# Performance work log

Hardware: AMD Instinct MI355X
Metric: run time of the kernel (lower is better)

Reference implementation:

```python
import jax, jax.numpy as jnp
import numpy as np

B, S, D = 4, 2048, 1024


def setup_inputs() -> dict:
    key = jax.random.key(0)
    ks = jax.random.split(key, 4)
    scale = 1.0 / np.sqrt(D)
    x = jax.random.normal(ks[0], (B, S, D), dtype=jnp.float32)
    Wk = jax.random.normal(ks[1], (D, D), dtype=jnp.float32) * scale
    Wq = jax.random.normal(ks[2], (D, D), dtype=jnp.float32) * scale
    Wv = jax.random.normal(ks[3], (D, D), dtype=jnp.float32) * scale
    bk = jnp.zeros((D,), dtype=jnp.float32)
    bq = jnp.zeros((D,), dtype=jnp.float32)
    bv = jnp.zeros((D,), dtype=jnp.float32)
    return {"x": x, "Wk": Wk, "bk": bk, "Wq": Wq, "bq": bq,
            "Wv": Wv, "bv": bv, "dims": 2}


def correlated_weight(k, q, v, dims):
    # correlation between every query position and every key position,
    # scaled by sqrt(d) for numerical stability (standard correlation attn)
    d = q.shape[-1]
    scores = jnp.einsum("bqd,bkd->bqk", q, k) / jnp.sqrt(jnp.asarray(d, q.dtype))
    w = jax.nn.softmax(scores, axis=dims)          # [B, S, S]
    return jnp.einsum("bqk,bkd->bqd", w, v)        # [B, S, D]


def reference(x, Wk, bk, Wq, bq, Wv, bv, dims):
    # injected key/query/value funcs instantiated as Linear layers
    k = jnp.einsum("bsd,de->bse", x, Wk) + bk
    q = jnp.einsum("bsd,de->bse", x, Wq) + bq
    v = jnp.einsum("bsd,de->bse", x, Wv) + bv
    return correlated_weight(k, q, v, dims)
```

## Files before the change

### kernel.cpp

```cpp
#include <hip/hip_runtime.h>
#include <hip/hip_bf16.h>
#include <stdint.h>


typedef unsigned short u16;
typedef __bf16 bf16x8 __attribute__((ext_vector_type(8)));
typedef float  f32x4  __attribute__((ext_vector_type(4)));
typedef float  f32x16 __attribute__((ext_vector_type(16)));
typedef u16    u16x4  __attribute__((ext_vector_type(4)));
typedef u16    u16x8  __attribute__((ext_vector_type(8)));

__device__ __forceinline__ u16 f2bf(float f) {
  union { float f; uint32_t u; } v; v.f = f;
  uint32_t r = v.u + 0x7fffu + ((v.u >> 16) & 1u);
  return (u16)(r >> 16);
}
__device__ __forceinline__ float bf2f(u16 b) {
  union { uint32_t u; float f; } v; v.u = (uint32_t)b << 16; return v.f;
}

#define GLD_LDS16(gp, lp) __builtin_amdgcn_global_load_lds(                   \
    (const __attribute__((address_space(1))) void*)(gp),                      \
    (__attribute__((address_space(3))) void*)(lp), 16, 0, 0)


__global__ __launch_bounds__(256)
void prep_all(const float* __restrict__ x,
              const float* __restrict__ Wq, const float* __restrict__ Wk,
              const float* __restrict__ Wv,
              const float* __restrict__ bq, const float* __restrict__ bk,
              const float* __restrict__ bv,
              u16* __restrict__ xb, u16* __restrict__ wt,
              float* __restrict__ bc) {
  __shared__ float t[32][33];
  const int bid = blockIdx.x;
  if (bid < 4096) {
    int i = (bid * 256 + threadIdx.x) * 8;
    float4 v0 = *(const float4*)(x + i);
    float4 v1 = *(const float4*)(x + i + 4);
    u16x8 o;
    o[0] = f2bf(v0.x); o[1] = f2bf(v0.y); o[2] = f2bf(v0.z); o[3] = f2bf(v0.w);
    o[4] = f2bf(v1.x); o[5] = f2bf(v1.y); o[6] = f2bf(v1.z); o[7] = f2bf(v1.w);
    *(u16x8*)(xb + i) = o;
  } else if (bid < 4096 + 3072) {
    int b2 = bid - 4096;
    int z = b2 >> 10, rem = b2 & 1023;
    int e0 = (rem & 31) * 32, d0 = (rem >> 5) * 32;
    const float* W = z == 0 ? Wq : (z == 1 ? Wk : Wv);
    u16* dst = wt + (size_t)z * 1024 * 1024;
    int tx = threadIdx.x & 31, ty = threadIdx.x >> 5;
    #pragma unroll
    for (int i = 0; i < 4; ++i)
      t[ty + i * 8][tx] = W[(size_t)(d0 + ty + i * 8) * 1024 + e0 + tx];
    __syncthreads();
    #pragma unroll
    for (int i = 0; i < 4; ++i)
      dst[(size_t)(e0 + ty + i * 8) * 1024 + d0 + tx] =
          f2bf(t[tx][ty + i * 8]);
  } else {
    int i = (bid - 7168) * 256 + threadIdx.x;
    if (i < 3072)
      bc[i] = (i < 1024) ? bq[i] : (i < 2048 ? bk[i - 1024] : bv[i - 2048]);
  }
}


__global__ __launch_bounds__(256)
void gemm_v(const u16* __restrict__ A, int lda,
            const u16* __restrict__ B, int ldb,
            const float* __restrict__ bias, int K,
            u16* __restrict__ vTp) {
  __shared__ __align__(16) u16 smem[128 * 132];
  u16* As = smem;
  u16* Bs = smem + 8192;
  const int lane = threadIdx.x & 63;
  const int wv = threadIdx.x >> 6;

  const int flat = blockIdx.y * 8 + blockIdx.x;
  const int swz = (flat & 7) * 64 + (flat >> 3);
  const int bx = swz & 7, by = swz >> 3;

  const u16* Ab = A + (size_t)by * 128 * lda;
  const u16* Bb = B + (size_t)bx * 128 * ldb;

  const int srow = lane >> 3;
  const int scol = ((lane & 7) ^ (lane >> 3)) * 8;
  const int r32 = lane & 31;
  const int half = lane >> 5;
  const int rx = lane & 7;
  const int wm = (wv >> 1) * 64;
  const int wn = (wv & 1) * 64;

  f32x16 acc[2][2];
  #pragma unroll
  for (int i = 0; i < 2; ++i)
    #pragma unroll
    for (int j = 0; j < 2; ++j) acc[i][j] = (f32x16)0.0f;

  for (int k0 = 0; k0 < K; k0 += 64) {
    #pragma unroll
    for (int i = 0; i < 4; ++i) {
      int r = wv * 32 + i * 8;
      GLD_LDS16(Ab + (size_t)(r + srow) * lda + k0 + scol, As + r * 64);
      GLD_LDS16(Bb + (size_t)(r + srow) * ldb + k0 + scol, Bs + r * 64);
    }
    __syncthreads();

    bf16x8 af[2][4], bfr[2][4];
    #pragma unroll
    for (int i = 0; i < 2; ++i)
      #pragma unroll
      for (int t = 0; t < 4; ++t) {
        int pc = ((t * 2 + half) ^ rx) * 8;
        af[i][t]  = *(const bf16x8*)(As + (wm + i * 32 + r32) * 64 + pc);
        bfr[i][t] = *(const bf16x8*)(Bs + (wn + i * 32 + r32) * 64 + pc);
      }
    #pragma unroll
    for (int i = 0; i < 2; ++i)
      #pragma unroll
      for (int j = 0; j < 2; ++j)
        #pragma unroll
        for (int t = 0; t < 4; ++t)
          acc[i][j] = __builtin_amdgcn_mfma_f32_32x32x16_bf16(
              af[i][t], bfr[j][t], acc[i][j], 0, 0, 0);
    __syncthreads();
  }

  u16 (*t)[132] = (u16(*)[132])smem;
  #pragma unroll
  for (int i = 0; i < 2; ++i) {
    #pragma unroll
    for (int j = 0; j < 2; ++j) {
      const int nl = wn + j * 32 + r32;
      const float bvv = bias[bx * 128 + nl];
      #pragma unroll
      for (int eg = 0; eg < 4; ++eg) {
        const int mb = wm + i * 32 + 4 * half + 8 * eg;
        u16x4 o;
        #pragma unroll
        for (int q = 0; q < 4; ++q) o[q] = f2bf(acc[i][j][eg * 4 + q] + bvv);
        *(u16x4*)&t[nl][mb] = o;
      }
    }
  }
  __syncthreads();
  const int tid = threadIdx.x;
  const int bb = by >> 4;
  const int s0 = (by & 15) * 128 + (tid & 15) * 8;
  const int e_base = bx * 128;
  u16* dstb = vTp + (size_t)bb * 1024 * 2048;
  #pragma unroll
  for (int p = 0; p < 8; ++p) {
    const int el = (tid >> 4) + p * 16;
    u16x8 o;
    #pragma unroll
    for (int q = 0; q < 8; ++q) o[q] = t[el][(tid & 15) * 8 + q];
    *(u16x8*)(dstb + (size_t)(e_base + el) * 2048 + s0) = o;
  }
}


#define FENCE8 asm volatile("" ::: "memory")
#define BARR8  do { FENCE8; __builtin_amdgcn_s_barrier(); FENCE8; } while (0)
#define WAITL8 asm volatile("s_waitcnt lgkmcnt(0)" ::: "memory")
#define VMW(N) asm volatile("s_waitcnt vmcnt(" #N ")" ::: "memory")

#define STAGE_A8(S, H, TT) do {                                               \
    GLD_LDS16(pA[H][0] + (TT) * 64,                                           \
              As + (S) * 16384 + ((H) * 64 + wv * 8) * 64);                   \
    GLD_LDS16(pA[H][1] + (TT) * 64,                                           \
              As + (S) * 16384 + ((H) * 64 + 128 + wv * 8) * 64);             \
  } while (0)

#define STAGE_B8(S, H, TT) do {                                               \
    GLD_LDS16(pB[H][0] + (TT) * 64,                                           \
              Bs + (S) * 16384 + ((H) * 32 + (wv >> 2) * 64 + (wv & 3) * 8) * 64); \
    GLD_LDS16(pB[H][1] + (TT) * 64,                                           \
              Bs + (S) * 16384 + ((H) * 32 + 128 + (wv >> 2) * 64 + (wv & 3) * 8) * 64); \
  } while (0)

#define RD_A8(S, MH) do {                                                     \
    _Pragma("unroll")                                                         \
    for (int mf = 0; mf < 4; ++mf) {                                          \
      const u16* p_ = As + (S) * 16384 + rdA + ((MH) * 64 + mf * 16) * 64;    \
      a[mf][0] = *(const bf16x8*)(p_ + pos0);                                 \
      a[mf][1] = *(const bf16x8*)(p_ + pos1);                                 \
    }                                                                         \
  } while (0)

#define RD_B8(S, NH) do {                                                     \
    _Pragma("unroll")                                                         \
    for (int nf = 0; nf < 2; ++nf) {                                          \
      const u16* p_ = Bs + (S) * 16384 + rdB + ((NH) * 32 + nf * 16) * 64;    \
      b[nf][0] = *(const bf16x8*)(p_ + pos0);                                 \
      b[nf][1] = *(const bf16x8*)(p_ + pos1);                                 \
    }                                                                         \
  } while (0)

#define MFMA_Q8(MH, NH) do {                                                  \
    _Pragma("unroll")                                                         \
    for (int ks = 0; ks < 2; ++ks)                                            \
      _Pragma("unroll")                                                       \
      for (int mf = 0; mf < 4; ++mf)                                          \
        _Pragma("unroll")                                                     \
        for (int nf = 0; nf < 2; ++nf)                                        \
          acc[(MH) * 4 + mf][(NH) * 2 + nf] =                                 \
              __builtin_amdgcn_mfma_f32_16x16x32_bf16(                        \
                  a[mf][ks], b[nf][ks], acc[(MH) * 4 + mf][(NH) * 2 + nf],    \
                  0, 0, 0);                                                   \
  } while (0)

#define GROUP8(S, T, EN1, EN2, WAITST) do {                                   \
    RD_A8(S, 0); RD_B8(S, 0);                                                 \
    if (EN1) STAGE_B8((S) ^ 1, 0, (T) + 1);                                   \
    BARR8; WAITL8;                                                            \
    __builtin_amdgcn_s_setprio(1); MFMA_Q8(0, 0);                             \
    __builtin_amdgcn_s_setprio(0); BARR8;                                     \
    RD_B8(S, 1);                                                              \
    if (EN2) STAGE_A8(S, 0, (T) + 2);                                         \
    BARR8; WAITL8;                                                            \
    __builtin_amdgcn_s_setprio(1); MFMA_Q8(0, 1);                             \
    __builtin_amdgcn_s_setprio(0); BARR8;                                     \
    RD_A8(S, 1);                                                              \
    if (EN2) STAGE_B8(S, 1, (T) + 2);                                         \
    BARR8; WAITL8;                                                            \
    __builtin_amdgcn_s_setprio(1); MFMA_Q8(1, 1);                             \
    __builtin_amdgcn_s_setprio(0); BARR8;                                     \
    RD_B8(S, 0);                                                              \
    if (EN2) STAGE_A8(S, 1, (T) + 2);                                         \
    BARR8; WAITL8;                                                            \
    __builtin_amdgcn_s_setprio(1); MFMA_Q8(1, 0);                             \
    __builtin_amdgcn_s_setprio(0); WAITST; BARR8;                             \
  } while (0)

template <int NT, bool OUT_BF16, bool BIAS>
__global__ __launch_bounds__(512)
void gemm8p(const u16* __restrict__ A, int lda, long long sA,
            const u16* __restrict__ B, int ldb, long long sB,
            void* __restrict__ C, int ldc, long long sC,
            const float* __restrict__ bias, float scale) {
  __shared__ __align__(16) u16 As[2 * 256 * 64];
  __shared__ __align__(16) u16 Bs[2 * 256 * 64];

  const int lane = threadIdx.x & 63;
  const int wv   = threadIdx.x >> 6;
  const int wm   = wv >> 2;
  const int wn   = wv & 3;
  const int l15  = lane & 15;
  const int hi4  = lane >> 4;
  const int rx7  = lane & 7;
  const int srow = lane >> 3;
  const int scem = ((lane & 7) ^ srow) * 8;

  const int nx = gridDim.x;
  const int flat = blockIdx.y * nx + blockIdx.x;
  const int nwg = nx * gridDim.y;
  const int cpx = nwg >> 3;
  const int swz = (flat & 7) * cpx + (flat >> 3);
  const int bx = swz % nx, by = swz / nx;

  const u16* Ab = A + (size_t)blockIdx.z * sA + (size_t)by * 256 * lda;
  const u16* Bb = B + (size_t)blockIdx.z * sB + (size_t)bx * 256 * ldb;

  const u16* pA[2][2];
  const u16* pB[2][2];
  #pragma unroll
  for (int h = 0; h < 2; ++h)
    #pragma unroll
    for (int r = 0; r < 2; ++r) {
      pA[h][r] = Ab + (size_t)(h * 64 + r * 128 + wv * 8 + srow) * lda + scem;
      pB[h][r] = Bb + (size_t)(h * 32 + r * 128 + (wv >> 2) * 64 +
                               (wv & 3) * 8 + srow) * ldb + scem;
    }

  const int rdA = (wm * 128 + l15) * 64;
  const int rdB = (wn * 64 + l15) * 64;
  const int pos0 = (hi4 ^ rx7) * 8;
  const int pos1 = ((4 + hi4) ^ rx7) * 8;

  f32x4 acc[8][4];
  #pragma unroll
  for (int i = 0; i < 8; ++i)
    #pragma unroll
    for (int j = 0; j < 4; ++j) acc[i][j] = (f32x4)0.0f;

  bf16x8 a[4][2], b[2][2];

  STAGE_A8(0, 0, 0); STAGE_B8(0, 1, 0); STAGE_A8(0, 1, 0); STAGE_B8(0, 0, 0);
  VMW(4);
  STAGE_A8(1, 0, 1); STAGE_B8(1, 1, 1); STAGE_A8(1, 1, 1);
  VMW(6);
  BARR8;

  #pragma unroll 1
  for (int i = 0; i < NT / 2 - 1; ++i) {
    const int t0 = 2 * i;
    GROUP8(0, t0,     1, 1, VMW(6));
    GROUP8(1, t0 + 1, 1, 1, VMW(6));
  }
  GROUP8(0, NT - 2, 1, 0, VMW(0));
  GROUP8(1, NT - 1, 0, 0, (void)0);

  const int m0 = by * 256 + wm * 128;
  const int n0 = bx * 256 + wn * 64;
  u16* Cb = (u16*)C + (size_t)blockIdx.z * sC;
  float* Cf = (float*)C + (size_t)blockIdx.z * sC;
  float bb[4];
  if (BIAS) {
    #pragma unroll
    for (int fn = 0; fn < 4; ++fn)
      bb[fn] = bias[n0 + (fn >> 1) * 32 + (fn & 1) * 16 + l15];
  }
  #pragma unroll
  for (int fm = 0; fm < 8; ++fm) {
    const int mb = m0 + (fm >> 2) * 64 + (fm & 3) * 16 + hi4 * 4;
    #pragma unroll
    for (int e = 0; e < 4; ++e) {
      const int m = mb + e;
      #pragma unroll
      for (int fn = 0; fn < 4; ++fn) {
        const int n = n0 + (fn >> 1) * 32 + (fn & 1) * 16 + l15;
        float v = acc[fm][fn][e] * scale;
        if (BIAS) v += bb[fn];
        if (OUT_BF16) Cb[(size_t)m * ldc + n] = f2bf(v);
        else          Cf[(size_t)m * ldc + n] = v;
      }
    }
  }
}


__global__ __launch_bounds__(512)
void gemm_bt8(const u16* __restrict__ A, int lda, long long sA,
              const u16* __restrict__ B, int ldb, long long sB,
              float* __restrict__ C, int ldc, long long sC,
              int K, float scale) {
  __shared__ u16 As[128 * 64];
  __shared__ u16 Bs[128 * 64];
  const int lane = threadIdx.x & 63;
  const int wv = threadIdx.x >> 6;

  const u16* Ab = A + (size_t)blockIdx.z * sA + (size_t)blockIdx.y * 128 * lda;
  const u16* Bb = B + (size_t)blockIdx.z * sB + (size_t)blockIdx.x * 128 * ldb;

  const int srow = lane >> 3;
  const int scol = ((lane & 7) ^ (lane >> 3)) * 8;
  const int r32 = lane & 31;
  const int half = lane >> 5;
  const int rx = lane & 7;
  const int wm = (wv >> 2) * 64;
  const int wn = (wv & 3) * 32;

  f32x16 acc[2];
  acc[0] = (f32x16)0.0f; acc[1] = (f32x16)0.0f;

  for (int k0 = 0; k0 < K; k0 += 64) {
    #pragma unroll
    for (int i = 0; i < 2; ++i) {
      int r = wv * 16 + i * 8;
      GLD_LDS16(Ab + (size_t)(r + srow) * lda + k0 + scol, As + r * 64);
      GLD_LDS16(Bb + (size_t)(r + srow) * ldb + k0 + scol, Bs + r * 64);
    }
    __syncthreads();

    bf16x8 af[2][4], bfr[4];
    #pragma unroll
    for (int t = 0; t < 4; ++t) {
      int pc = ((t * 2 + half) ^ rx) * 8;
      af[0][t] = *(const bf16x8*)(As + (wm + r32) * 64 + pc);
      af[1][t] = *(const bf16x8*)(As + (wm + 32 + r32) * 64 + pc);
      bfr[t]   = *(const bf16x8*)(Bs + (wn + r32) * 64 + pc);
    }
    #pragma unroll
    for (int i = 0; i < 2; ++i)
      #pragma unroll
      for (int t = 0; t < 4; ++t)
        acc[i] = __builtin_amdgcn_mfma_f32_32x32x16_bf16(
            af[i][t], bfr[t], acc[i], 0, 0, 0);
    __syncthreads();
  }

  const int ccol = blockIdx.x * 128 + wn + r32;
  const int crow0 = blockIdx.y * 128 + wm + 4 * half;
  float* Cf = C + (size_t)blockIdx.z * sC;
  #pragma unroll
  for (int i = 0; i < 2; ++i)
    #pragma unroll
    for (int e = 0; e < 16; ++e) {
      int m = crow0 + i * 32 + (e & 3) + 8 * (e >> 2);
      Cf[(size_t)m * ldc + ccol] = acc[i][e] * scale;
    }
}


__global__ __launch_bounds__(256) void softmax_rows(u16* __restrict__ P) {
  __shared__ float red[4];
  const int t = threadIdx.x;
  const int lane = t & 63, wv = t >> 6;
  u16* row = P + (size_t)blockIdx.x * 2048;
  u16x8 w = ((const u16x8*)row)[t];
  float v[8];
  #pragma unroll
  for (int j = 0; j < 8; ++j) v[j] = bf2f(w[j]);
  float m = v[0];
  #pragma unroll
  for (int j = 1; j < 8; ++j) m = fmaxf(m, v[j]);
  #pragma unroll
  for (int off = 32; off > 0; off >>= 1) m = fmaxf(m, __shfl_down(m, off));
  if (lane == 0) red[wv] = m;
  __syncthreads();
  m = fmaxf(fmaxf(red[0], red[1]), fmaxf(red[2], red[3]));
  __syncthreads();
  float e[8], s = 0.f;
  #pragma unroll
  for (int j = 0; j < 8; ++j) { e[j] = exp2f((v[j] - m) * 1.44269504f); s += e[j]; }
  #pragma unroll
  for (int off = 32; off > 0; off >>= 1) s += __shfl_down(s, off);
  if (lane == 0) red[wv] = s;
  __syncthreads();
  s = red[0] + red[1] + red[2] + red[3];
  float inv = 1.0f / s;
  u16x8 o;
  #pragma unroll
  for (int j = 0; j < 8; ++j) o[j] = f2bf(e[j] * inv);
  ((u16x8*)row)[t] = o;
}


extern "C" void kernel_launch(void* const* d_in, const int* in_sizes, int n_in,
                              void* d_out, int out_size, void* d_ws, size_t ws_size,
                              hipStream_t stream) {
  const float* x  = (const float*)d_in[0];
  const float* Wk = (const float*)d_in[1];
  const float* bk = (const float*)d_in[2];
  const float* Wq = (const float*)d_in[3];
  const float* bq = (const float*)d_in[4];
  const float* Wv = (const float*)d_in[5];
  const float* bv = (const float*)d_in[6];
  float* out = (float*)d_out;

  char* ws = (char*)d_ws;
  u16*   xb  = (u16*)(ws + 0);
  u16*   wt  = (u16*)(ws + 16777216);
  float* bc  = (float*)(ws + 23068672);
  u16*   qk  = (u16*)(ws + 23080960);
  u16*   vT  = (u16*)(ws + 56635392);
  u16*   P   = (u16*)(ws + 73412608);
  (void)in_sizes; (void)n_in; (void)out_size; (void)ws_size;

  prep_all<<<7180, 256, 0, stream>>>(x, Wq, Wk, Wv, bq, bk, bv, xb, wt, bc);

  gemm8p<16, true, true><<<dim3(8, 32, 1), 512, 0, stream>>>(
      xb, 1024, 0LL, wt, 1024, 0LL, (void*)qk, 2048, 0LL, bc, 1.0f);

  gemm_v<<<dim3(8, 64, 1), 256, 0, stream>>>(
      xb, 1024, wt + 2048 * 1024, 1024, bc + 2048, 1024, vT);

  gemm8p<16, true, false><<<dim3(8, 8, 4), 512, 0, stream>>>(
      qk, 2048, 2048LL * 2048, qk + 1024, 2048, 2048LL * 2048,
      (void*)P, 2048, 2048LL * 2048, nullptr, 0.03125f);

  softmax_rows<<<8192, 256, 0, stream>>>(P);

  gemm_bt8<<<dim3(8, 16, 4), 512, 0, stream>>>(
      P, 2048, 2048LL * 2048, vT, 2048, 1024LL * 2048,
      out, 1024, 2048LL * 1024, 2048, 1.0f);
}
```

Baseline: 257.6 us.

## Prefetch next-stage LDS fragments into double register sets in 8-wave GEMM

Reworks the 8-wave GEMM main loop so LDS fragment reads for the next k-tile's first quadrant are issued during the last quadrant of the current tile, into separate register buffers (a0/a1, b1, and ping-pong bcA/bcB). LDS reads become inline ds_read_b128 asm with partial lgkmcnt waits and sched_barrier, so MFMAs can start while later reads are still in flight. This aims to hide LDS read latency behind MFMA work. The cost is more VGPR pressure and more delicate wait-count correctness, and the global stage order and vmcnt thresholds change with it.

Result: slower. 325.2 us (+26.2%).

```diff
diff --git a/kernel.cpp b/kernel.cpp
--- a/kernel.cpp
+++ b/kernel.cpp
@@ -4,7 +4,9 @@
 
 
 typedef unsigned short u16;
+typedef uint32_t u32;
 typedef __bf16 bf16x8 __attribute__((ext_vector_type(8)));
+typedef u32    u32x4  __attribute__((ext_vector_type(4)));
 typedef float  f32x4  __attribute__((ext_vector_type(4)));
 typedef float  f32x16 __attribute__((ext_vector_type(16)));
 typedef u16    u16x4  __attribute__((ext_vector_type(4)));
@@ -162,8 +164,15 @@
 
 #define FENCE8 asm volatile("" ::: "memory")
 #define BARR8  do { FENCE8; __builtin_amdgcn_s_barrier(); FENCE8; } while (0)
-#define WAITL8 asm volatile("s_waitcnt lgkmcnt(0)" ::: "memory")
 #define VMW(N) asm volatile("s_waitcnt vmcnt(" #N ")" ::: "memory")
+#define LGK(N) asm volatile("s_waitcnt lgkmcnt(" #N ")" ::: "memory")
+#define SBAR0  __builtin_amdgcn_sched_barrier(0)
+
+#define DSR(DST, PTR) asm volatile("ds_read_b128 %0, %1"                      \
+    : "=v"(DST)                                                               \
+    : "v"((unsigned)(uintptr_t)                                               \
+          (__attribute__((address_space(3))) const void*)(PTR))               \
+    : "memory")
 
 #define STAGE_A8(S, H, TT) do {                                               \
     GLD_LDS16(pA[H][0] + (TT) * 64,                                           \
@@ -179,25 +188,25 @@
               Bs + (S) * 16384 + ((H) * 32 + 128 + (wv >> 2) * 64 + (wv & 3) * 8) * 64); \
   } while (0)
 
-#define RD_A8(S, MH) do {                                                     \
+#define RD_A(S, MH, DST) do {                                                 \
     _Pragma("unroll")                                                         \
     for (int mf = 0; mf < 4; ++mf) {                                          \
       const u16* p_ = As + (S) * 16384 + rdA + ((MH) * 64 + mf * 16) * 64;    \
-      a[mf][0] = *(const bf16x8*)(p_ + pos0);                                 \
-      a[mf][1] = *(const bf16x8*)(p_ + pos1);                                 \
+      DSR(DST[mf][0], p_ + pos0);                                             \
+      DSR(DST[mf][1], p_ + pos1);                                             \
     }                                                                         \
   } while (0)
 
-#define RD_B8(S, NH) do {                                                     \
+#define RD_B(S, NH, DST) do {                                                 \
     _Pragma("unroll")                                                         \
     for (int nf = 0; nf < 2; ++nf) {                                          \
       const u16* p_ = Bs + (S) * 16384 + rdB + ((NH) * 32 + nf * 16) * 64;    \
-      b[nf][0] = *(const bf16x8*)(p_ + pos0);                                 \
-      b[nf][1] = *(const bf16x8*)(p_ + pos1);                                 \
+      DSR(DST[nf][0], p_ + pos0);                                             \
+      DSR(DST[nf][1], p_ + pos1);                                             \
     }                                                                         \
   } while (0)
 
-#define MFMA_Q8(MH, NH) do {                                                  \
+#define MFMAQ(MH, NH, AR, BR) do {                                            \
     _Pragma("unroll")                                                         \
     for (int ks = 0; ks < 2; ++ks)                                            \
       _Pragma("unroll")                                                       \
@@ -206,39 +215,43 @@
         for (int nf = 0; nf < 2; ++nf)                                        \
           acc[(MH) * 4 + mf][(NH) * 2 + nf] =                                 \
               __builtin_amdgcn_mfma_f32_16x16x32_bf16(                        \
-                  a[mf][ks], b[nf][ks], acc[(MH) * 4 + mf][(NH) * 2 + nf],    \
-                  0, 0, 0);                                                   \
-  } while (0)
-
-#define GROUP8(S, T, EN1, EN2, WAITST) do {                                   \
-    RD_A8(S, 0); RD_B8(S, 0);                                                 \
+                  __builtin_bit_cast(bf16x8, AR[mf][ks]),                     \
+                  __builtin_bit_cast(bf16x8, BR[nf][ks]),                     \
+                  acc[(MH) * 4 + mf][(NH) * 2 + nf], 0, 0, 0);                \
+  } while (0)
+
+#define GROUPR(S, T, BC, BN, EN1, EN2, EN4R, W3) do {                         \
+                                                                     \
+    RD_B(S, 1, b1);                                                           \
     if (EN1) STAGE_B8((S) ^ 1, 0, (T) + 1);                                   \
-    BARR8; WAITL8;                                                            \
-    __builtin_amdgcn_s_setprio(1); MFMA_Q8(0, 0);                             \
+    BARR8; LGK(4); SBAR0;                                                     \
+    __builtin_amdgcn_s_setprio(1); MFMAQ(0, 0, a0, BC);                       \
     __builtin_amdgcn_s_setprio(0); BARR8;                                     \
-    RD_B8(S, 1);                                                              \
+                                                                     \
+    RD_A(S, 1, a1);                                                           \
     if (EN2) STAGE_A8(S, 0, (T) + 2);                                         \
-    BARR8; WAITL8;                                                            \
-    __builtin_amdgcn_s_setprio(1); MFMA_Q8(0, 1);                             \
+    BARR8; LGK(8); SBAR0;                                                     \
+    __builtin_amdgcn_s_setprio(1); MFMAQ(0, 1, a0, b1);                       \
     __builtin_amdgcn_s_setprio(0); BARR8;                                     \
-    RD_A8(S, 1);                                                              \
+     \
     if (EN2) STAGE_B8(S, 1, (T) + 2);                                         \
-    BARR8; WAITL8;                                                            \
-    __builtin_amdgcn_s_setprio(1); MFMA_Q8(1, 1);                             \
+    BARR8; LGK(0); SBAR0;                                                     \
+    __builtin_amdgcn_s_setprio(1); MFMAQ(1, 1, a1, b1);                       \
+    __builtin_amdgcn_s_setprio(0); W3; BARR8;                                 \
+                                                                     \
+    if (EN4R) { RD_A((S) ^ 1, 0, a0); RD_B((S) ^ 1, 0, BN); }                 \
+    if (EN2) STAGE_A8(S, 1, (T) + 2);                                         \
+    BARR8; SBAR0;                                                             \
+    __builtin_amdgcn_s_setprio(1); MFMAQ(1, 0, a1, BC);                       \
     __builtin_amdgcn_s_setprio(0); BARR8;                                     \
-    RD_B8(S, 0);                                                              \
-    if (EN2) STAGE_A8(S, 1, (T) + 2);                                         \
-    BARR8; WAITL8;                                                            \
-    __builtin_amdgcn_s_setprio(1); MFMA_Q8(1, 0);                             \
-    __builtin_amdgcn_s_setprio(0); WAITST; BARR8;                             \
   } while (0)
 
 template <int NT, bool OUT_BF16, bool BIAS>
 __global__ __launch_bounds__(512)
-void gemm8p(const u16* __restrict__ A, int lda, long long sA,
-            const u16* __restrict__ B, int ldb, long long sB,
-            void* __restrict__ C, int ldc, long long sC,
-            const float* __restrict__ bias, float scale) {
+void gemm8r2(const u16* __restrict__ A, int lda, long long sA,
+             const u16* __restrict__ B, int ldb, long long sB,
+             void* __restrict__ C, int ldc, long long sC,
+             const float* __restrict__ bias, float scale) {
   __shared__ __align__(16) u16 As[2 * 256 * 64];
   __shared__ __align__(16) u16 Bs[2 * 256 * 64];
 
@@ -284,22 +297,21 @@
     #pragma unroll
     for (int j = 0; j < 4; ++j) acc[i][j] = (f32x4)0.0f;
 
-  bf16x8 a[4][2], b[2][2];
-
-  STAGE_A8(0, 0, 0); STAGE_B8(0, 1, 0); STAGE_A8(0, 1, 0); STAGE_B8(0, 0, 0);
-  VMW(4);
+  u32x4 a0[4][2], a1[4][2], b1[2][2], bcA[2][2], bcB[2][2];
+
+  STAGE_A8(0, 0, 0); STAGE_B8(0, 0, 0); STAGE_B8(0, 1, 0); STAGE_A8(0, 1, 0);
   STAGE_A8(1, 0, 1); STAGE_B8(1, 1, 1); STAGE_A8(1, 1, 1);
   VMW(6);
   BARR8;
+  RD_A(0, 0, a0); RD_B(0, 0, bcA);
 
   #pragma unroll 1
   for (int i = 0; i < NT / 2 - 1; ++i) {
-    const int t0 = 2 * i;
-    GROUP8(0, t0,     1, 1, VMW(6));
-    GROUP8(1, t0 + 1, 1, 1, VMW(6));
-  }
-  GROUP8(0, NT - 2, 1, 0, VMW(0));
-  GROUP8(1, NT - 1, 0, 0, (void)0);
+    GROUPR(0, 2 * i,     bcA, bcB, 1, 1, 1, VMW(4));
+    GROUPR(1, 2 * i + 1, bcB, bcA, 1, 1, 1, VMW(4));
+  }
+  GROUPR(0, NT - 2, bcA, bcB, 1, 0, 1, VMW(0));
+  GROUPR(1, NT - 1, bcB, bcA, 0, 0, 0, (void)0);
 
   const int m0 = by * 256 + wm * 128;
   const int n0 = bx * 256 + wn * 64;
@@ -450,13 +462,13 @@
 
   prep_all<<<7180, 256, 0, stream>>>(x, Wq, Wk, Wv, bq, bk, bv, xb, wt, bc);
 
-  gemm8p<16, true, true><<<dim3(8, 32, 1), 512, 0, stream>>>(
+  gemm8r2<16, true, true><<<dim3(8, 32, 1), 512, 0, stream>>>(
       xb, 1024, 0LL, wt, 1024, 0LL, (void*)qk, 2048, 0LL, bc, 1.0f);
 
   gemm_v<<<dim3(8, 64, 1), 256, 0, stream>>>(
       xb, 1024, wt + 2048 * 1024, 1024, bc + 2048, 1024, vT);
 
-  gemm8p<16, true, false><<<dim3(8, 8, 4), 512, 0, stream>>>(
+  gemm8r2<16, true, false><<<dim3(8, 8, 4), 512, 0, stream>>>(
       qk, 2048, 2048LL * 2048, qk + 1024, 2048, 2048LL * 2048,
       (void*)P, 2048, 2048LL * 2048, nullptr, 0.03125f);
 
```
